# Optimization experiments

Measured on AMD Instinct MI355X. Metric: run time of the kernel, lower is better.

The kernel has to match this reference:

```python
import jax, jax.numpy as jnp
import numpy as np

B, PLEN, D = 32, 1024, 256


def setup_inputs() -> dict:
    key = jax.random.key(0)
    ks = jax.random.split(key, 8)
    u = lambda k, shape: jax.random.uniform(k, shape, jnp.float32, -0.05, 0.05)
    return {
        "P": jax.random.normal(ks[0], (B, PLEN, D), jnp.float32),
        "w_itr_att": u(ks[1], (3 * D,)),
        "w1": u(ks[2], (2 * D, D)),
        "w2": u(ks[3], (2 * D, D)),
        "w3": u(ks[4], (2 * D, D)),
        "b1": u(ks[5], (D,)),
        "b2": u(ks[6], (D,)),
        "b3": u(ks[7], (D,)),
    }


def reference(P, w_itr_att, w1, w2, w3, b1, b2, b3):
    d = P.shape[-1]
    # alpha(a,b) = w_itr_att . [a ; b ; a*b]; split w into the three d-chunks
    wa, wb, wc = w_itr_att[:d], w_itr_att[d:2 * d], w_itr_att[2 * d:]
    # pairwise score A[b,i,j] = wa.P_i + wb.P_j + wc.(P_i * P_j)
    sa = P @ wa                                   # (b, p)
    sb = P @ wb                                   # (b, p)
    A = sa[:, :, None] + sb[:, None, :] + jnp.einsum('bid,bjd->bij', P * wc, P)
    itr_attn = jnp.einsum('bij,bjd->bid', jax.nn.softmax(A, axis=2), P)
    cat = jnp.concatenate([P, itr_attn], axis=-1)  # (b, p, 2d)
    z = jnp.tanh(cat @ w1 + b1)
    r = jax.nn.sigmoid(cat @ w2 + b2)
    f = jax.nn.sigmoid(cat @ w3 + b3)
    return r * P + f * z
```

## Files before the change

kernel.cpp:

```cpp
#include <hip/hip_runtime.h>
#include <hip/hip_bf16.h>

typedef unsigned short u16;
typedef unsigned int   u32;

using bf16x8 = __attribute__((ext_vector_type(8))) short;
using f32x4  = __attribute__((ext_vector_type(4))) float;

#define NB 32
#define NP 1024
#define ND 256

__device__ __forceinline__ u16 f2bf(float x){
  u32 u = __float_as_uint(x);
  u += 0x7FFFu + ((u >> 16) & 1u);
  return (u16)(u >> 16);
}

__device__ __forceinline__ float bf2f(u16 x){
  return __uint_as_float((u32)x << 16);
}

__device__ __forceinline__ void glds16(const void* g, void* l){
  __builtin_amdgcn_global_load_lds((const __attribute__((address_space(1))) void*)g,
                                   (__attribute__((address_space(3))) void*)l, 16, 0, 0);
}

__global__ void prep_rows(const float* __restrict__ P, const float* __restrict__ wi,
                          u16* __restrict__ Pbf, float* __restrict__ sbv){
  const int row  = blockIdx.x * 4 + (threadIdx.x >> 6);
  const int lane = threadIdx.x & 63;
  const float4 p  = *(const float4*)(P  + (size_t)row * ND + lane * 4);
  const float4 wb = *(const float4*)(wi + ND + lane * 4);
  ushort4 pb;
  pb.x = f2bf(p.x); pb.y = f2bf(p.y); pb.z = f2bf(p.z); pb.w = f2bf(p.w);
  *(ushort4*)(Pbf + (size_t)row * ND + lane * 4) = pb;
  float s = p.x*wb.x + p.y*wb.y + p.z*wb.z + p.w*wb.w;
  #pragma unroll
  for (int m = 1; m < 64; m <<= 1) s += __shfl_xor(s, m, 64);
  if (lane == 0) sbv[row] = s;
}

__global__ void prep_w(const float* __restrict__ w1, const float* __restrict__ w2,
                       const float* __restrict__ w3, u16* __restrict__ Wp){
  const int t = blockIdx.x;
  const float* w = (t < 16) ? w1 : ((t < 32) ? w2 : w3);
  const int tid = threadIdx.x;
  #pragma unroll
  for (int j = 0; j < 4; ++j){
    int item = tid + 256 * j;
    int c = item >> 6, lane = item & 63;
    int ncol = ((t & 15) << 4) + (lane & 15);
    int k0 = 32 * c + 8 * (lane >> 4);
    u16 tmp[8];
    #pragma unroll
    for (int e = 0; e < 8; ++e) tmp[e] = f2bf(w[(size_t)(k0 + e) * 256 + ncol]);
    *(uint4*)(Wp + ((size_t)(t * 16 + c) * 64 + lane) * 8) = *(uint4*)tmp;
  }
}

__global__ void transpose_p(const u16* __restrict__ Pbf, u16* __restrict__ PbfT){
  const int b = blockIdx.z, jt = blockIdx.x, dt = blockIdx.y;
  __shared__ u16 T[64][72];
  const int tid = threadIdx.x;
  #pragma unroll
  for (int it = 0; it < 2; ++it){
    int cc = tid + 256 * it;
    int j = cc >> 3, c8 = cc & 7;
    uint4 v = *(const uint4*)(Pbf + ((size_t)b * NP + jt * 64 + j) * ND + dt * 64 + c8 * 8);
    *(uint4*)&T[j][c8 * 8] = v;
  }
  __syncthreads();
  #pragma unroll
  for (int it = 0; it < 2; ++it){
    int cc = tid + 256 * it;
    int d = cc >> 3, c8 = cc & 7;
    u16 tmp[8];
    #pragma unroll
    for (int k = 0; k < 8; ++k) tmp[k] = T[c8 * 8 + k][d];
    *(uint4*)(PbfT + ((size_t)b * ND + dt * 64 + d) * NP + jt * 64 + c8 * 8) = *(uint4*)tmp;
  }
}

__launch_bounds__(256, 2)
__global__ void attn_kernel(const float* __restrict__ P, const float* __restrict__ wi,
                            const u16* __restrict__ Pbf, const u16* __restrict__ PbfT,
                            const float* __restrict__ sbv, u16* __restrict__ attnb){
  const int bid  = ((blockIdx.x & 7) << 6) | (blockIdx.x >> 3);
  const int b    = bid >> 4;
  const int q0   = (bid & 15) << 6;
  const int tid  = threadIdx.x;
  const int wave = tid >> 6, lane = tid & 63, lo = lane & 15, hi = lane >> 4;

  __shared__ __align__(16) u16 KtA[64 * 256];
  __shared__ __align__(16) u16 VtA[256 * 64];
  __shared__ __align__(16) u16 Sp[4][16][72];
  __shared__ float sbt[64];
  char* KtB = (char*)KtA;
  char* VtB = (char*)VtA;

  bf16x8 qf[8];
  {
    const int qrow = q0 + wave * 16 + lo;
    const float* prow = P  + ((size_t)b * NP + qrow) * ND;
    const float* wcp  = wi + 512;
    #pragma unroll
    for (int c = 0; c < 8; ++c){
      const int d0 = 32 * c + 8 * hi;
      float4 a  = *(const float4*)(prow + d0);
      float4 a2 = *(const float4*)(prow + d0 + 4);
      float4 wa  = *(const float4*)(wcp + d0);
      float4 wa2 = *(const float4*)(wcp + d0 + 4);
      bf16x8 q;
      q[0]=(short)f2bf(a.x*wa.x);  q[1]=(short)f2bf(a.y*wa.y);
      q[2]=(short)f2bf(a.z*wa.z);  q[3]=(short)f2bf(a.w*wa.w);
      q[4]=(short)f2bf(a2.x*wa2.x); q[5]=(short)f2bf(a2.y*wa2.y);
      q[6]=(short)f2bf(a2.z*wa2.z); q[7]=(short)f2bf(a2.w*wa2.w);
      qf[c] = q;
    }
  }

  f32x4 of[16];
  #pragma unroll
  for (int t = 0; t < 16; ++t) of[t] = (f32x4){0.f,0.f,0.f,0.f};
  float mx[4] = {-1e30f,-1e30f,-1e30f,-1e30f};
  float ls[4] = {0.f,0.f,0.f,0.f};

  const u16* kslab = Pbf  + (size_t)b * NP * ND;
  const u16* vslab = PbfT + (size_t)b * ND * NP;

  for (int kt = 0; kt < 16; ++kt){
    const int kbase = kt * 64;

    #pragma unroll
    for (int it = 0; it < 8; ++it){
      int off = it * 4096 + wave * 1024 + lane * 16;
      int row = off >> 9;
      int cl  = (off & 511) ^ ((row & 7) << 4);
      const char* g = (const char*)(kslab + (size_t)(kbase + row) * ND) + cl;
      glds16(g, KtB + it * 4096 + wave * 1024);
    }
    #pragma unroll
    for (int it = 0; it < 8; ++it){
      int off = it * 4096 + wave * 1024 + lane * 16;
      int d   = off >> 7;
      int cl  = (off & 127) ^ ((d & 7) << 4);
      const char* g = (const char*)(vslab + (size_t)d * NP + kbase) + cl;
      glds16(g, VtB + it * 4096 + wave * 1024);
    }
    if (tid < 64) sbt[tid] = sbv[(size_t)b * NP + kbase + tid];
    __syncthreads();

    f32x4 s[4];
    #pragma unroll
    for (int nt = 0; nt < 4; ++nt){
      f32x4 acc = (f32x4){0.f,0.f,0.f,0.f};
      #pragma unroll
      for (int c = 0; c < 8; ++c){
        int row = nt * 16 + lo;
        int pb  = row * 512 + ((64 * c + 16 * hi) ^ ((row & 7) << 4));
        bf16x8 kf = *(const bf16x8*)(KtB + pb);
        acc = __builtin_amdgcn_mfma_f32_16x16x32_bf16(qf[c], kf, acc, 0, 0, 0);
      }
      s[nt] = acc;
    }
    #pragma unroll
    for (int nt = 0; nt < 4; ++nt){
      float sv = sbt[nt * 16 + lo];
      #pragma unroll
      for (int r = 0; r < 4; ++r) s[nt][r] += sv;
    }

    float scale[4];
    #pragma unroll
    for (int r = 0; r < 4; ++r){
      float v = fmaxf(fmaxf(s[0][r], s[1][r]), fmaxf(s[2][r], s[3][r]));
      v = fmaxf(v, __shfl_xor(v, 1, 64));
      v = fmaxf(v, __shfl_xor(v, 2, 64));
      v = fmaxf(v, __shfl_xor(v, 4, 64));
      v = fmaxf(v, __shfl_xor(v, 8, 64));
      float mnew = fmaxf(mx[r], v);
      scale[r] = __expf(mx[r] - mnew);
      mx[r] = mnew;
      float rs = 0.f;
      #pragma unroll
      for (int nt = 0; nt < 4; ++nt){
        float p = __expf(s[nt][r] - mnew);
        s[nt][r] = p; rs += p;
      }
      rs += __shfl_xor(rs, 1, 64);
      rs += __shfl_xor(rs, 2, 64);
      rs += __shfl_xor(rs, 4, 64);
      rs += __shfl_xor(rs, 8, 64);
      ls[r] = ls[r] * scale[r] + rs;
    }
    #pragma unroll
    for (int t = 0; t < 16; ++t){
      #pragma unroll
      for (int r = 0; r < 4; ++r) of[t][r] *= scale[r];
    }
    #pragma unroll
    for (int nt = 0; nt < 4; ++nt)
      #pragma unroll
      for (int r = 0; r < 4; ++r)
        Sp[wave][4 * hi + r][16 * nt + lo] = f2bf(s[nt][r]);

    #pragma unroll
    for (int kk = 0; kk < 2; ++kk){
      bf16x8 pa = *(const bf16x8*)&Sp[wave][lo][32 * kk + 8 * hi];
      #pragma unroll
      for (int t = 0; t < 16; ++t){
        int d  = 16 * t + lo;
        int pb = d * 128 + ((64 * kk + 16 * hi) ^ ((d & 7) << 4));
        bf16x8 vb = *(const bf16x8*)(VtB + pb);
        of[t] = __builtin_amdgcn_mfma_f32_16x16x32_bf16(pa, vb, of[t], 0, 0, 0);
      }
    }
    __syncthreads();
  }

  const int qrow = q0 + wave * 16;
  #pragma unroll
  for (int t = 0; t < 16; ++t){
    #pragma unroll
    for (int r = 0; r < 4; ++r){
      float o = of[t][r] / ls[r];
      attnb[((size_t)b * NP + qrow + 4 * hi + r) * ND + 16 * t + lo] = f2bf(o);
    }
  }
}

__launch_bounds__(256, 2)
__global__ void mlp_kernel(const u16* __restrict__ Pbf, const u16* __restrict__ attnb,
                           const u16* __restrict__ Wp,
                           const float* __restrict__ b1, const float* __restrict__ b2,
                           const float* __restrict__ b3, float* __restrict__ out){
  const int p    = blockIdx.x;
  const int swz  = ((p & 7) << 7) | (p >> 3);
  const int mt   = swz >> 2, cg = swz & 3;
  const int tid  = threadIdx.x;
  const int wave = tid >> 6, lane = tid & 63, lo = lane & 15, hi = lane >> 4;
  const int tq   = 4 * cg + wave;
  const int m0   = mt * 128;

  __shared__ __align__(16) u16 Ab[2][128 * 64];

  f32x4 acc[3][8];
  #pragma unroll
  for (int e = 0; e < 3; ++e)
    #pragma unroll
    for (int m = 0; m < 8; ++m) acc[e][m] = (f32x4){0.f,0.f,0.f,0.f};

  auto stage = [&](int s, int buf){
    const u16* xs = (s < 4) ? (Pbf   + (size_t)m0 * ND + s * 64)
                            : (attnb + (size_t)m0 * ND + (s - 4) * 64);
    char* dst = (char*)Ab[buf];
    #pragma unroll
    for (int it = 0; it < 4; ++it){
      int off = it * 4096 + wave * 1024 + lane * 16;
      int row = off >> 7;
      int cl  = (off & 127) ^ ((row & 7) << 4);
      glds16((const char*)(xs + (size_t)row * ND) + cl, dst + it * 4096 + wave * 1024);
    }
  };

  stage(0, 0);
  __syncthreads();

  for (int s = 0; s < 8; ++s){
    if (s < 7) stage(s + 1, (s + 1) & 1);
    const char* ab = (const char*)Ab[s & 1];
    #pragma unroll
    for (int cc = 0; cc < 2; ++cc){
      const int c = 2 * s + cc;
      bf16x8 wf[3];
      #pragma unroll
      for (int e = 0; e < 3; ++e)
        wf[e] = *(const bf16x8*)(Wp + ((size_t)((tq + 16 * e) * 16 + c) * 64 + lane) * 8);
      #pragma unroll
      for (int m = 0; m < 8; ++m){
        int row = 16 * m + lo;
        bf16x8 af = *(const bf16x8*)(ab + row * 128 + ((64 * cc + 16 * hi) ^ ((row & 7) << 4)));
        #pragma unroll
        for (int e = 0; e < 3; ++e)
          acc[e][m] = __builtin_amdgcn_mfma_f32_16x16x32_bf16(af, wf[e], acc[e][m], 0, 0, 0);
      }
    }
    __syncthreads();
  }

  const int d = 16 * tq + lo;
  const float bb1 = b1[d], bb2 = b2[d], bb3 = b3[d];
  #pragma unroll
  for (int m = 0; m < 8; ++m){
    #pragma unroll
    for (int r = 0; r < 4; ++r){
      const int row = m0 + 16 * m + 4 * hi + r;
      float y1 = acc[0][m][r] + bb1;
      float y2 = acc[1][m][r] + bb2;
      float y3 = acc[2][m][r] + bb3;
      float pv = bf2f(Pbf[(size_t)row * ND + d]);
      float e2 = __expf(2.f * y1);
      float z  = (e2 - 1.f) / (e2 + 1.f);
      float rr = 1.f / (1.f + __expf(-y2));
      float ff = 1.f / (1.f + __expf(-y3));
      out[(size_t)row * ND + d] = rr * pv + ff * z;
    }
  }
}

extern "C" void kernel_launch(void* const* d_in, const int* in_sizes, int n_in,
                              void* d_out, int out_size, void* d_ws, size_t ws_size,
                              hipStream_t stream){
  const float* P  = (const float*)d_in[0];
  const float* wi = (const float*)d_in[1];
  const float* w1 = (const float*)d_in[2];
  const float* w2 = (const float*)d_in[3];
  const float* w3 = (const float*)d_in[4];
  const float* b1 = (const float*)d_in[5];
  const float* b2 = (const float*)d_in[6];
  const float* b3 = (const float*)d_in[7];
  float* out = (float*)d_out;

  char* ws = (char*)d_ws;
  u16*   Pbf   = (u16*)  (ws);
  u16*   PbfT  = (u16*)  (ws + (16u << 20));
  u16*   attnb = (u16*)  (ws + (32u << 20));
  u16*   Wp    = (u16*)  (ws + (48u << 20));
  float* sbv   = (float*)(ws + (49u << 20));

  prep_rows<<<8192, 256, 0, stream>>>(P, wi, Pbf, sbv);
  prep_w<<<48, 256, 0, stream>>>(w1, w2, w3, Wp);
  transpose_p<<<dim3(16, 4, 32), 256, 0, stream>>>(Pbf, PbfT);
  attn_kernel<<<512, 256, 0, stream>>>(P, wi, Pbf, PbfT, sbv, attnb);
  mlp_kernel<<<1024, 256, 0, stream>>>(Pbf, attnb, Wp, b1, b2, b3, out);
}
```

Before: 126.7 us.

## Double-buffer K/V tiles in attention with 512-thread blocks over 128 query rows

The attention kernel now runs 256 blocks of 8 waves, each covering 128 query rows, so each staged K/V tile is reused by twice as many waves. K and V tiles are double-buffered in LDS and the next tile is prefetched with global_load_lds while the current one is computed, leaving one barrier per iteration. The LDS layout switches to a chunk-major arrangement with a different XOR swizzle, and the sb bias is prefetched into registers instead of shared memory. The cost is twice the LDS per block and one block per CU, and the grid now has exactly 256 blocks, which may leave CUs idle with no tail to fill.

New measurement: 133.0 us. 4.9% more time.

```diff
diff --git a/kernel.cpp b/kernel.cpp
--- a/kernel.cpp
+++ b/kernel.cpp
@@ -82,22 +82,20 @@
   }
 }
 
-__launch_bounds__(256, 2)
+__launch_bounds__(512, 1)
 __global__ void attn_kernel(const float* __restrict__ P, const float* __restrict__ wi,
                             const u16* __restrict__ Pbf, const u16* __restrict__ PbfT,
                             const float* __restrict__ sbv, u16* __restrict__ attnb){
-  const int bid  = ((blockIdx.x & 7) << 6) | (blockIdx.x >> 3);
-  const int b    = bid >> 4;
-  const int q0   = (bid & 15) << 6;
+  const int p    = blockIdx.x;
+  const int bid  = ((p & 7) << 5) | (p >> 3);
+  const int b    = bid >> 3;
+  const int q0   = (bid & 7) << 7;
   const int tid  = threadIdx.x;
   const int wave = tid >> 6, lane = tid & 63, lo = lane & 15, hi = lane >> 4;
 
-  __shared__ __align__(16) u16 KtA[64 * 256];
-  __shared__ __align__(16) u16 VtA[256 * 64];
-  __shared__ __align__(16) u16 Sp[4][16][72];
-  __shared__ float sbt[64];
-  char* KtB = (char*)KtA;
-  char* VtB = (char*)VtA;
+  __shared__ __align__(16) u16 KtA[2][16384];
+  __shared__ __align__(16) u16 VtA[2][16384];
+  __shared__ __align__(16) u16 Sp[8][16][72];
 
   bf16x8 qf[8];
   {
@@ -129,27 +127,42 @@
   const u16* kslab = Pbf  + (size_t)b * NP * ND;
   const u16* vslab = PbfT + (size_t)b * ND * NP;
 
+  auto stageKV = [&](int kt, int buf){
+    const int kbase = kt * 64;
+    char* KtB = (char*)KtA[buf];
+    char* VtB = (char*)VtA[buf];
+    #pragma unroll
+    for (int r = 0; r < 4; ++r){
+      int off = r * 8192 + tid * 16;
+      int ck  = off >> 10;
+      int row = ((off >> 4) & 63) ^ ((ck & 1) << 4);
+      glds16((const char*)(kslab + (size_t)(kbase + row) * ND + ck * 8), KtB + off);
+    }
+    #pragma unroll
+    for (int r = 0; r < 4; ++r){
+      int off = r * 8192 + tid * 16;
+      int c   = off >> 12;
+      int d   = ((off >> 4) & 255) ^ ((c & 1) << 4);
+      glds16((const char*)(vslab + (size_t)d * NP + kbase + c * 8), VtB + off);
+    }
+  };
+
+  float sbc[4], sbn[4];
+  stageKV(0, 0);
+  #pragma unroll
+  for (int nt = 0; nt < 4; ++nt) sbc[nt] = sbv[(size_t)b * NP + nt * 16 + lo];
+  __syncthreads();
+
   for (int kt = 0; kt < 16; ++kt){
-    const int kbase = kt * 64;
-
-    #pragma unroll
-    for (int it = 0; it < 8; ++it){
-      int off = it * 4096 + wave * 1024 + lane * 16;
-      int row = off >> 9;
-      int cl  = (off & 511) ^ ((row & 7) << 4);
-      const char* g = (const char*)(kslab + (size_t)(kbase + row) * ND) + cl;
-      glds16(g, KtB + it * 4096 + wave * 1024);
-    }
-    #pragma unroll
-    for (int it = 0; it < 8; ++it){
-      int off = it * 4096 + wave * 1024 + lane * 16;
-      int d   = off >> 7;
-      int cl  = (off & 127) ^ ((d & 7) << 4);
-      const char* g = (const char*)(vslab + (size_t)d * NP + kbase) + cl;
-      glds16(g, VtB + it * 4096 + wave * 1024);
-    }
-    if (tid < 64) sbt[tid] = sbv[(size_t)b * NP + kbase + tid];
-    __syncthreads();
+    const int cur = kt & 1;
+    if (kt < 15){
+      stageKV(kt + 1, cur ^ 1);
+      #pragma unroll
+      for (int nt = 0; nt < 4; ++nt)
+        sbn[nt] = sbv[(size_t)b * NP + (kt + 1) * 64 + nt * 16 + lo];
+    }
+    const char* KtB = (const char*)KtA[cur];
+    const char* VtB = (const char*)VtA[cur];
 
     f32x4 s[4];
     #pragma unroll
@@ -157,16 +170,13 @@
       f32x4 acc = (f32x4){0.f,0.f,0.f,0.f};
       #pragma unroll
       for (int c = 0; c < 8; ++c){
-        int row = nt * 16 + lo;
-        int pb  = row * 512 + ((64 * c + 16 * hi) ^ ((row & 7) << 4));
-        bf16x8 kf = *(const bf16x8*)(KtB + pb);
+        int ck = 4 * c + hi;
+        int ad = ck * 1024 + ((((nt << 4) + lo) ^ ((ck & 1) << 4)) << 4);
+        bf16x8 kf = *(const bf16x8*)(KtB + ad);
         acc = __builtin_amdgcn_mfma_f32_16x16x32_bf16(qf[c], kf, acc, 0, 0, 0);
       }
       s[nt] = acc;
-    }
-    #pragma unroll
-    for (int nt = 0; nt < 4; ++nt){
-      float sv = sbt[nt * 16 + lo];
+      float sv = sbc[nt];
       #pragma unroll
       for (int r = 0; r < 4; ++r) s[nt][r] += sv;
     }
@@ -185,8 +195,8 @@
       float rs = 0.f;
       #pragma unroll
       for (int nt = 0; nt < 4; ++nt){
-        float p = __expf(s[nt][r] - mnew);
-        s[nt][r] = p; rs += p;
+        float pv = __expf(s[nt][r] - mnew);
+        s[nt][r] = pv; rs += pv;
       }
       rs += __shfl_xor(rs, 1, 64);
       rs += __shfl_xor(rs, 2, 64);
@@ -208,15 +218,17 @@
     #pragma unroll
     for (int kk = 0; kk < 2; ++kk){
       bf16x8 pa = *(const bf16x8*)&Sp[wave][lo][32 * kk + 8 * hi];
+      int c = 4 * kk + hi;
+      int cb = c * 4096, cs = (c & 1) << 4;
       #pragma unroll
       for (int t = 0; t < 16; ++t){
-        int d  = 16 * t + lo;
-        int pb = d * 128 + ((64 * kk + 16 * hi) ^ ((d & 7) << 4));
-        bf16x8 vb = *(const bf16x8*)(VtB + pb);
+        int ad = cb + ((((t << 4) + lo) ^ cs) << 4);
+        bf16x8 vb = *(const bf16x8*)(VtB + ad);
         of[t] = __builtin_amdgcn_mfma_f32_16x16x32_bf16(pa, vb, of[t], 0, 0, 0);
       }
     }
-    __syncthreads();
+    sbc[0] = sbn[0]; sbc[1] = sbn[1]; sbc[2] = sbn[2]; sbc[3] = sbn[3];
+    if (kt < 15) __syncthreads();
   }
 
   const int qrow = q0 + wave * 16;
@@ -332,6 +344,6 @@
   prep_rows<<<8192, 256, 0, stream>>>(P, wi, Pbf, sbv);
   prep_w<<<48, 256, 0, stream>>>(w1, w2, w3, Wp);
   transpose_p<<<dim3(16, 4, 32), 256, 0, stream>>>(Pbf, PbfT);
-  attn_kernel<<<512, 256, 0, stream>>>(P, wi, Pbf, PbfT, sbv, attnb);
+  attn_kernel<<<256, 512, 0, stream>>>(P, wi, Pbf, PbfT, sbv, attnb);
   mlp_kernel<<<1024, 256, 0, stream>>>(Pbf, attnb, Wp, b1, b2, b3, out);
 }
```
